# Optimization experiments

Hardware: AMD Instinct MI355X
Metric: run time of the kernel (lower is better)

## Reference

```python
import jax, jax.numpy as jnp
import numpy as np
from jax.scipy.special import logsumexp

TEMPERATURE = 0.1
BETA = 0.999
EPS = 1e-8
HARD_K = 10  # min(num_classes // 4, 10) with num_classes = 1000


def _l2norm(x, axis=-1):
    return x * jax.lax.rsqrt(jnp.sum(x * x, axis=axis, keepdims=True) + 1e-24)


def setup_inputs() -> dict:
    key = jax.random.key(0)
    k1, k2, k3, k4, k5 = jax.random.split(key, 5)
    B, D, C, M = 4096, 1024, 1000, 32768
    return {
        "image_features": jax.random.normal(k1, (B, D), dtype=jnp.float32),
        "prompts": jax.random.normal(k2, (C, D), dtype=jnp.float32),
        "labels": jax.random.randint(k3, (B, C), 0, 2, dtype=jnp.int32),
        "memory_features": jax.random.normal(k4, (M, D), dtype=jnp.float32),
        "memory_labels": jax.random.randint(k5, (M, C), 0, 2, dtype=jnp.int32),
        "mem_ptr": 16384,
    }


def reference(image_features, prompts, labels, memory_features, memory_labels, mem_ptr):
    B, D = image_features.shape
    C = prompts.shape[0]
    labels_f = labels.astype(jnp.float32)

    # z_img = F.normalize(image_features)
    z_img = _l2norm(image_features, axis=1)

    # class weights (effective-number reweighting), computed from this batch's labels
    counts = labels_f.sum(axis=0)                              # [C]
    effective_num = 1.0 - jnp.power(jnp.float32(BETA), counts)
    weights = (1.0 - BETA) / (effective_num + EPS)
    weights = weights / jnp.sum(weights) * C                   # [C]

    # memory bank update (detached write of current batch at ptr), then use [:ptr+B]
    mem_f = memory_features.at[mem_ptr:mem_ptr + B].set(jax.lax.stop_gradient(z_img))
    mem_l = memory_labels.at[mem_ptr:mem_ptr + B].set(labels)
    used = mem_ptr + B  # static

    enhanced_features = jnp.concatenate([z_img, mem_f[:used]], axis=0)     # [N, D]
    enhanced_labels = jnp.concatenate([labels_f, mem_l[:used].astype(jnp.float32)], axis=0)  # [N, C]

    z_prompts = _l2norm(prompts, axis=1)                       # [C, D]
    sim = (enhanced_features @ z_prompts.T) / TEMPERATURE      # [N, C]

    pos_mask = enhanced_labels > 0                             # [N, C]

    # hard negatives: top-K similarities among negatives define the keep threshold
    sim_for_neg = jnp.where(pos_mask, -jnp.inf, sim)
    hard_neg_vals, _ = jax.lax.top_k(sim_for_neg, HARD_K)      # [N, K]
    min_hard_neg = hard_neg_vals[:, -1:]                       # [N, 1]
    neg_mask = (~pos_mask) & (sim >= min_hard_neg)
    full_mask = pos_mask | neg_mask

    lse = logsumexp(jnp.where(full_mask, sim, -jnp.inf), axis=1)  # [N]
    log_prob = sim - lse[:, None]                              # [N, C]

    posf = pos_mask.astype(sim.dtype)
    pos_w = posf * weights[None, :]                            # [N, C]
    weight_sums = pos_w.sum(axis=1)                            # [N]
    loss_num = (pos_w * (-log_prob)).sum(axis=1)               # [N]

    valid = weight_sums > 0
    loss_per_sample = jnp.where(valid, loss_num / (weight_sums + EPS), 0.0)
    n_valid = jnp.maximum(valid.sum(), 1)
    attr_loss = loss_per_sample.sum() / n_valid.astype(sim.dtype)
    # single attribute -> total_loss / num_valid_attrs == attr_loss
    return attr_loss
```

## Files before the change

kernel.cpp:

```cpp
#include <hip/hip_runtime.h>
#include <math.h>

#define BN    4096
#define DD    1024
#define CC    1000
#define MM    32768
#define ROWS_CAP 32768
#define SIMLD 1024


#define NGROUP_A 512
#define NGROUP_B 16
#define NCOUNT   512

typedef __attribute__((ext_vector_type(8))) int   int8v;
typedef __attribute__((ext_vector_type(16))) float f32x16;

__device__ __forceinline__ float wave_max_f(float v) {
#pragma unroll
  for (int off = 32; off >= 1; off >>= 1) v = fmaxf(v, __shfl_xor(v, off, 64));
  return v;
}
__device__ __forceinline__ float wave_sum_f(float v) {
#pragma unroll
  for (int off = 32; off >= 1; off >>= 1) v += __shfl_xor(v, off, 64);
  return v;
}

__device__ __forceinline__ short f2bf(float f) {
  union { float f; unsigned u; } v; v.f = f;
  unsigned r = v.u + 0x7FFF + ((v.u >> 16) & 1);
  return (short)(r >> 16);
}
__device__ __forceinline__ float bf2f(unsigned short u) {
  union { unsigned u; float f; } v; v.u = ((unsigned)u) << 16;
  return v.f;
}

__device__ __forceinline__ int pack4(float a, float b, float c, float d) {
  int p = __builtin_amdgcn_cvt_pk_fp8_f32(a, b, 0, false);
  p = __builtin_amdgcn_cvt_pk_fp8_f32(c, d, p, true);
  return p;
}

__device__ __forceinline__ void gload16(const unsigned char* g, unsigned char* l) {
  __builtin_amdgcn_global_load_lds(
      (const __attribute__((address_space(1))) unsigned int*)g,
      (__attribute__((address_space(3))) unsigned int*)l, 16, 0, 0);
}

__global__ __launch_bounds__(256) void conv_kernel(const float* __restrict__ img,
                                                   const float* __restrict__ prompts,
                                                   const float* __restrict__ mem,
                                                   const int* __restrict__ memptr,
                                                   unsigned char* __restrict__ A,
                                                   unsigned char* __restrict__ B,
                                                   const int* __restrict__ labels,
                                                   int* __restrict__ counts) {
  const int blk = blockIdx.x;

  if (blk >= NGROUP_A + NGROUP_B) {
    const int ci = blk - (NGROUP_A + NGROUP_B);
    const int c = (ci & 3) * 256 + threadIdx.x;
    if (c >= CC) return;
    const int b0 = (ci >> 2) * 32;
    int s = 0;
#pragma unroll
    for (int b = 0; b < 32; ++b) s += labels[(size_t)(b0 + b) * CC + c];
    atomicAdd(&counts[c], s);
    return;
  }

  __shared__ unsigned char tile[65536];
  const int t = threadIdx.x;
  const int lane = t & 63;
  const int wid = t >> 6;
  const int nrows = BN + memptr[0];
  const int padded = (nrows + 127) & ~127;

  const bool isB = (blk >= NGROUP_A);
  const int g = isB ? (blk - NGROUP_A) : blk;
  const int rowBase = g * 64;
  if (!isB && rowBase >= padded) return;

  unsigned char* dstBase = (isB ? B : A)
      + (size_t)(rowBase >> 7) * 131072 + (size_t)(rowBase & 64) * 16;

  for (int i = 0; i < 16; ++i) {
    const int r = wid * 16 + i;
    const int row = rowBase + r;
    const float* src = nullptr;
    float esc = 1.0f;
    bool needNorm = false;
    if (isB) {
      if (row < CC) { src = prompts + (size_t)row * DD; needNorm = true; esc = 10.0f; }
    } else {
      if (row < BN)         { src = img + (size_t)row * DD; needNorm = true; }
      else if (row < nrows) { src = mem + (size_t)(row - BN) * DD; }
    }
    int4 o = {0, 0, 0, 0};
    if (src) {
      const float4* s4 = (const float4*)src + lane * 4;
      float4 a = s4[0], b = s4[1], c = s4[2], d = s4[3];
      float sc = esc;
      if (needNorm) {
        float ss = a.x * a.x + a.y * a.y + a.z * a.z + a.w * a.w
                 + b.x * b.x + b.y * b.y + b.z * b.z + b.w * b.w
                 + c.x * c.x + c.y * c.y + c.z * c.z + c.w * c.w
                 + d.x * d.x + d.y * d.y + d.z * d.z + d.w * d.w;
        ss = wave_sum_f(ss);
        sc = esc * rsqrtf(ss + 1e-24f);
      }
      o.x = pack4(a.x * sc, a.y * sc, a.z * sc, a.w * sc);
      o.y = pack4(b.x * sc, b.y * sc, b.z * sc, b.w * sc);
      o.z = pack4(c.x * sc, c.y * sc, c.z * sc, c.w * sc);
      o.w = pack4(d.x * sc, d.y * sc, d.z * sc, d.w * sc);
    }
    *(int4*)(tile + lane * 1024 + (((r + lane) & 63) << 4)) = o;
  }
  __syncthreads();

#pragma unroll
  for (int p = 0; p < 16; ++p) {
    const int ochunk = p * 256 + t;
    const int kc = ochunk >> 6;
    const int rl = ochunk & 63;
    int4 v = *(const int4*)(tile + kc * 1024 + (((rl + kc) & 63) << 4));
    *(int4*)(dstBase + (size_t)kc * 2048 + rl * 16) = v;
  }
}

__global__ __launch_bounds__(256) void gemm_mx(const unsigned char* __restrict__ A,
                                               const unsigned char* __restrict__ Bm,
                                               const int* __restrict__ memptr,
                                               short* __restrict__ simbf, int lo) {
  const int f = blockIdx.x;
  const int x = f & 7;
  const int s = f >> 3;
  const int c = s & 7;
  const int rt = (s >> 3) * 8 + x;

  const int nrows = BN + memptr[0];
  const int row0 = rt * 128;
  if (lo + row0 >= nrows) return;
  const int c0 = c * 128;

  __shared__ unsigned char As[16384];
  __shared__ unsigned char Bs[16384];

  const int t = threadIdx.x;
  const int lane = t & 63;
  const int wid = t >> 6;
  const int wm = (wid >> 1) * 64;
  const int wn = (wid & 1) * 64;

  const unsigned char* gaT = A + (size_t)(lo + row0) * DD;
  const unsigned char* gbT = Bm + (size_t)c0 * DD;
  unsigned char* lA = As + t * 16;
  unsigned char* lB = Bs + t * 16;

  f32x16 acc[2][2] = {};
  const int q = lane >> 5;
  const int rr = lane & 31;

  for (int k0 = 0; k0 < DD; k0 += 128) {
    const size_t kb = (size_t)k0 * 128;
#pragma unroll
    for (int p = 0; p < 4; ++p)
      gload16(gaT + kb + p * 4096 + t * 16, lA + p * 4096);
#pragma unroll
    for (int p = 0; p < 4; ++p)
      gload16(gbT + kb + p * 4096 + t * 16, lB + p * 4096);
    __syncthreads();
#pragma unroll
    for (int h = 0; h < 2; ++h) {
      int8v af[2], bfv[2];
      const int kc = h * 4 + q * 2;
#pragma unroll
      for (int mi = 0; mi < 2; ++mi) {
        const unsigned char* pa = As + kc * 2048 + (wm + mi * 32 + rr) * 16;
        int4 lo4 = *(const int4*)pa;
        int4 hi4 = *(const int4*)(pa + 2048);
        af[mi][0] = lo4.x; af[mi][1] = lo4.y; af[mi][2] = lo4.z; af[mi][3] = lo4.w;
        af[mi][4] = hi4.x; af[mi][5] = hi4.y; af[mi][6] = hi4.z; af[mi][7] = hi4.w;
      }
#pragma unroll
      for (int ni = 0; ni < 2; ++ni) {
        const unsigned char* pb = Bs + kc * 2048 + (wn + ni * 32 + rr) * 16;
        int4 lo4 = *(const int4*)pb;
        int4 hi4 = *(const int4*)(pb + 2048);
        bfv[ni][0] = lo4.x; bfv[ni][1] = lo4.y; bfv[ni][2] = lo4.z; bfv[ni][3] = lo4.w;
        bfv[ni][4] = hi4.x; bfv[ni][5] = hi4.y; bfv[ni][6] = hi4.z; bfv[ni][7] = hi4.w;
      }
#pragma unroll
      for (int mi = 0; mi < 2; ++mi)
#pragma unroll
        for (int ni = 0; ni < 2; ++ni)
          acc[mi][ni] = __builtin_amdgcn_mfma_scale_f32_32x32x64_f8f6f4(
              af[mi], bfv[ni], acc[mi][ni], 0, 0, 0, 127, 0, 127);
    }
    __syncthreads();
  }

  const int cl = lane & 31;
  const int r4 = 4 * (lane >> 5);
#pragma unroll
  for (int mi = 0; mi < 2; ++mi)
#pragma unroll
    for (int ni = 0; ni < 2; ++ni) {
      f32x16 v = acc[mi][ni];
      const int colg = c0 + wn + ni * 32 + cl;
      const int rbase = row0 + wm + mi * 32 + r4;
#pragma unroll
      for (int reg = 0; reg < 16; ++reg) {
        const int rowl = rbase + (reg & 3) + 8 * (reg >> 2);
        simbf[(size_t)rowl * SIMLD + colg] = f2bf(v[reg]);
      }
    }
}

__global__ __launch_bounds__(256) void rowpost_kernel(
    const short* __restrict__ simbf, const int* __restrict__ labels,
    const int* __restrict__ mlabels, const int* __restrict__ counts,
    const int* __restrict__ memptr, float* __restrict__ lps_arr,
    float* __restrict__ valid_arr, int chunk_lo) {
  __shared__ float wlds[1024];
  __shared__ float wpart[4];
  {
    const int t = threadIdx.x;
    float wv[4];
    float acc = 0.f;
#pragma unroll
    for (int i = 0; i < 4; ++i) {
      int c = t + i * 256;
      float w = 0.f;
      if (c < CC) {
        float cnt = (float)counts[c];
        float en = 1.0f - expf(cnt * logf(0.999f));
        w = (1.0f - 0.999f) / (en + 1e-8f);
      }
      wv[i] = w;
      acc += w;
    }
    float s = wave_sum_f(acc);
    if ((t & 63) == 0) wpart[t >> 6] = s;
    __syncthreads();
    float tot = wpart[0] + wpart[1] + wpart[2] + wpart[3];
    float sc = (float)CC / tot;
#pragma unroll
    for (int i = 0; i < 4; ++i) wlds[t + i * 256] = wv[i] * sc;
    __syncthreads();
  }

  const int nrows = BN + memptr[0];
  const int wid = threadIdx.x >> 6;
  const int lane = threadIdx.x & 63;
  const int row = chunk_lo + blockIdx.x * 4 + wid;
  if (row >= ROWS_CAP) return;
  if (row >= nrows) {
    if (lane == 0) { lps_arr[row] = 0.f; valid_arr[row] = 0.f; }
    return;
  }

  const unsigned short* srow = (const unsigned short*)simbf + (size_t)(row - chunk_lo) * SIMLD;
  const int* lrow = (row < BN) ? labels + (size_t)row * CC
                               : mlabels + (size_t)(row - BN) * CC;
  const int cbase = lane * 16;

  unsigned short sraw[16];
  *(ulonglong2*)&sraw[0] = *(const ulonglong2*)(srow + cbase);
  *(ulonglong2*)&sraw[8] = *(const ulonglong2*)(srow + cbase + 8);
  int lab[16];
#pragma unroll
  for (int g = 0; g < 4; ++g) {
    int c = cbase + g * 4;
    if (c + 3 < CC) {
      *(int4*)&lab[g * 4] = *(const int4*)(lrow + c);
    } else {
#pragma unroll
      for (int u = 0; u < 4; ++u) lab[g * 4 + u] = (c + u < CC) ? lrow[c + u] : 0;
    }
  }

  float sv[16];
  bool pv[16];
  float vneg[16];
#pragma unroll
  for (int j = 0; j < 16; ++j) {
    int c = cbase + j;
    bool ok = (c < CC);
    float sf = bf2f(sraw[j]);
    bool p = ok && (lab[j] > 0);
    sv[j] = ok ? sf : -INFINITY;
    pv[j] = p;
    vneg[j] = (ok && !p) ? sf : -INFINITY;
  }

  float v10 = -INFINITY;
  for (int r = 0; r < 10; ++r) {
    float lmx = -INFINITY;
#pragma unroll
    for (int j = 0; j < 16; ++j) lmx = fmaxf(lmx, vneg[j]);
    lmx = wave_max_f(lmx);
#pragma unroll
    for (int j = 0; j < 16; ++j) if (vneg[j] == lmx) vneg[j] = -INFINITY;
    v10 = lmx;
  }

  float mmax = -INFINITY;
#pragma unroll
  for (int j = 0; j < 16; ++j) {
    if (pv[j] || sv[j] >= v10) mmax = fmaxf(mmax, sv[j]);
  }
  mmax = wave_max_f(mmax);

  float esum = 0.f, wsum = 0.f, wsim = 0.f;
#pragma unroll
  for (int j = 0; j < 16; ++j) {
    int c = cbase + j;
    if (c < CC) {
      if (pv[j] || sv[j] >= v10) esum += expf(sv[j] - mmax);
      if (pv[j]) { float w = wlds[c]; wsum += w; wsim += w * sv[j]; }
    }
  }
  esum = wave_sum_f(esum);
  wsum = wave_sum_f(wsum);
  wsim = wave_sum_f(wsim);

  if (lane == 0) {
    float lse = mmax + logf(esum);
    bool valid = (wsum > 0.f);
    float lps = valid ? (wsum * lse - wsim) / (wsum + 1e-8f) : 0.f;
    float mult = (row < BN) ? 2.f : 1.f;
    lps_arr[row] = mult * lps;
    valid_arr[row] = valid ? mult : 0.f;
  }
}

__global__ __launch_bounds__(1024) void reduce_kernel(const float* __restrict__ lps_arr,
                                                      const float* __restrict__ valid_arr,
                                                      float* __restrict__ out) {
  const int t = threadIdx.x;
  const float4* l4 = (const float4*)lps_arr;
  const float4* v4 = (const float4*)valid_arr;
  float s1 = 0.f, s2 = 0.f;
#pragma unroll
  for (int i = 0; i < 8; ++i) {
    float4 a = l4[t + i * 1024];
    float4 b = v4[t + i * 1024];
    s1 += a.x + a.y + a.z + a.w;
    s2 += b.x + b.y + b.z + b.w;
  }
  s1 = wave_sum_f(s1);
  s2 = wave_sum_f(s2);
  __shared__ float p1[16], p2[16];
  if ((t & 63) == 0) { p1[t >> 6] = s1; p2[t >> 6] = s2; }
  __syncthreads();
  if (t == 0) {
    float a = 0.f, b = 0.f;
#pragma unroll
    for (int i = 0; i < 16; ++i) { a += p1[i]; b += p2[i]; }
    out[0] = a / fmaxf(b, 1.0f);
  }
}

extern "C" void kernel_launch(void* const* d_in, const int* in_sizes, int n_in,
                              void* d_out, int out_size, void* d_ws, size_t ws_size,
                              hipStream_t stream) {
  const float* img     = (const float*)d_in[0];
  const float* prompts = (const float*)d_in[1];
  const int*   labels  = (const int*)d_in[2];
  const float* mem     = (const float*)d_in[3];
  const int*   mlabels = (const int*)d_in[4];
  const int*   memptr  = (const int*)d_in[5];
  float* out = (float*)d_out;
  char* ws = (char*)d_ws;

  int*   counts  = (int*)(ws + 0);
  float* lps_arr = (float*)(ws + 8192);
  float* val_arr = (float*)(ws + 139264);
  unsigned char* Bf8 = (unsigned char*)(ws + 270336);
  unsigned char* Af8 = (unsigned char*)(ws + 1318912);
  const size_t fixed = 1318912 + (size_t)ROWS_CAP * DD;
  short* simbf = (short*)(ws + fixed);

  long long avail = (long long)ws_size - (long long)fixed;
  int chunk = (int)(avail / (SIMLD * 2));
  chunk &= ~1023;
  if (chunk < 1024) chunk = 1024;
  if (chunk > ROWS_CAP) chunk = ROWS_CAP;

  hipMemsetAsync(ws, 0, 4096, stream);

  conv_kernel<<<NGROUP_A + NGROUP_B + NCOUNT, 256, 0, stream>>>(
      img, prompts, mem, memptr, Af8, Bf8, labels, counts);

  for (int lo = 0; lo < ROWS_CAP; lo += chunk) {
    int rows = (ROWS_CAP - lo < chunk) ? (ROWS_CAP - lo) : chunk;
    int rowTiles = rows / 128;
    gemm_mx<<<8 * rowTiles, 256, 0, stream>>>(Af8, Bf8, memptr, simbf, lo);
    rowpost_kernel<<<rows / 4, 256, 0, stream>>>(simbf, labels, mlabels, counts, memptr,
                                                 lps_arr, val_arr, lo);
  }
  reduce_kernel<<<1, 1024, 0, stream>>>(lps_arr, val_arr, out);
}
```

Baseline: 331.6 us.

## Fuse row post-processing into GEMM epilogue with per-tile partial top-k merging

Removes the bf16 similarity matrix round-trip by computing per-tile partial statistics in the GEMM epilogue: a running top-10 of negatives via med3 insertion, the positive max, exp-sum and weighted sums. Each row gets 32 column-slice partials, and a new merge kernel combines them with online logsumexp. Labels are packed into LDS bitmasks and the class weights are recomputed per block. This also drops the chunked loop, but writes 14x32 floats of partials per row and lengthens the epilogue, which raises register pressure.

Measured after the change: 420.9 us. +26.9%, slower.

```diff
diff --git a/kernel.cpp b/kernel.cpp
--- a/kernel.cpp
+++ b/kernel.cpp
@@ -6,35 +6,21 @@
 #define CC    1000
 #define MM    32768
 #define ROWS_CAP 32768
-#define SIMLD 1024
 
 
 #define NGROUP_A 512
 #define NGROUP_B 16
 #define NCOUNT   512
 
+#define NSUB 32
+
 typedef __attribute__((ext_vector_type(8))) int   int8v;
 typedef __attribute__((ext_vector_type(16))) float f32x16;
 
-__device__ __forceinline__ float wave_max_f(float v) {
-#pragma unroll
-  for (int off = 32; off >= 1; off >>= 1) v = fmaxf(v, __shfl_xor(v, off, 64));
-  return v;
-}
 __device__ __forceinline__ float wave_sum_f(float v) {
 #pragma unroll
   for (int off = 32; off >= 1; off >>= 1) v += __shfl_xor(v, off, 64);
   return v;
-}
-
-__device__ __forceinline__ short f2bf(float f) {
-  union { float f; unsigned u; } v; v.f = f;
-  unsigned r = v.u + 0x7FFF + ((v.u >> 16) & 1);
-  return (short)(r >> 16);
-}
-__device__ __forceinline__ float bf2f(unsigned short u) {
-  union { unsigned u; float f; } v; v.u = ((unsigned)u) << 16;
-  return v.f;
 }
 
 __device__ __forceinline__ int pack4(float a, float b, float c, float d) {
@@ -47,6 +33,12 @@
   __builtin_amdgcn_global_load_lds(
       (const __attribute__((address_space(1))) unsigned int*)g,
       (__attribute__((address_space(3))) unsigned int*)l, 16, 0, 0);
+}
+
+__device__ __forceinline__ void ins10(float* t, float v) {
+#pragma unroll
+  for (int i = 9; i >= 1; --i) t[i] = __builtin_amdgcn_fmed3f(v, t[i - 1], t[i]);
+  t[0] = fmaxf(t[0], v);
 }
 
 __global__ __launch_bounds__(256) void conv_kernel(const float* __restrict__ img,
@@ -130,23 +122,29 @@
   }
 }
 
-__global__ __launch_bounds__(256) void gemm_mx(const unsigned char* __restrict__ A,
-                                               const unsigned char* __restrict__ Bm,
-                                               const int* __restrict__ memptr,
-                                               short* __restrict__ simbf, int lo) {
+__global__ __launch_bounds__(256) void gemm_fused(const unsigned char* __restrict__ A,
+                                                  const unsigned char* __restrict__ Bm,
+                                                  const int* __restrict__ labels,
+                                                  const int* __restrict__ mlabels,
+                                                  const int* __restrict__ counts,
+                                                  const int* __restrict__ memptr,
+                                                  float* __restrict__ partials) {
   const int f = blockIdx.x;
   const int x = f & 7;
   const int s = f >> 3;
-  const int c = s & 7;
+  const int cb = s & 7;
   const int rt = (s >> 3) * 8 + x;
 
   const int nrows = BN + memptr[0];
   const int row0 = rt * 128;
-  if (lo + row0 >= nrows) return;
-  const int c0 = c * 128;
+  if (row0 >= nrows) return;
+  const int c0 = cb * 128;
 
   __shared__ unsigned char As[16384];
   __shared__ unsigned char Bs[16384];
+  __shared__ unsigned posbits[128][4];
+  __shared__ float wcol[128];
+  __shared__ float wpart[4];
 
   const int t = threadIdx.x;
   const int lane = t & 63;
@@ -154,82 +152,9 @@
   const int wm = (wid >> 1) * 64;
   const int wn = (wid & 1) * 64;
 
-  const unsigned char* gaT = A + (size_t)(lo + row0) * DD;
-  const unsigned char* gbT = Bm + (size_t)c0 * DD;
-  unsigned char* lA = As + t * 16;
-  unsigned char* lB = Bs + t * 16;
-
-  f32x16 acc[2][2] = {};
-  const int q = lane >> 5;
-  const int rr = lane & 31;
-
-  for (int k0 = 0; k0 < DD; k0 += 128) {
-    const size_t kb = (size_t)k0 * 128;
-#pragma unroll
-    for (int p = 0; p < 4; ++p)
-      gload16(gaT + kb + p * 4096 + t * 16, lA + p * 4096);
-#pragma unroll
-    for (int p = 0; p < 4; ++p)
-      gload16(gbT + kb + p * 4096 + t * 16, lB + p * 4096);
-    __syncthreads();
-#pragma unroll
-    for (int h = 0; h < 2; ++h) {
-      int8v af[2], bfv[2];
-      const int kc = h * 4 + q * 2;
-#pragma unroll
-      for (int mi = 0; mi < 2; ++mi) {
-        const unsigned char* pa = As + kc * 2048 + (wm + mi * 32 + rr) * 16;
-        int4 lo4 = *(const int4*)pa;
-        int4 hi4 = *(const int4*)(pa + 2048);
-        af[mi][0] = lo4.x; af[mi][1] = lo4.y; af[mi][2] = lo4.z; af[mi][3] = lo4.w;
-        af[mi][4] = hi4.x; af[mi][5] = hi4.y; af[mi][6] = hi4.z; af[mi][7] = hi4.w;
-      }
-#pragma unroll
-      for (int ni = 0; ni < 2; ++ni) {
-        const unsigned char* pb = Bs + kc * 2048 + (wn + ni * 32 + rr) * 16;
-        int4 lo4 = *(const int4*)pb;
-        int4 hi4 = *(const int4*)(pb + 2048);
-        bfv[ni][0] = lo4.x; bfv[ni][1] = lo4.y; bfv[ni][2] = lo4.z; bfv[ni][3] = lo4.w;
-        bfv[ni][4] = hi4.x; bfv[ni][5] = hi4.y; bfv[ni][6] = hi4.z; bfv[ni][7] = hi4.w;
-      }
-#pragma unroll
-      for (int mi = 0; mi < 2; ++mi)
-#pragma unroll
-        for (int ni = 0; ni < 2; ++ni)
-          acc[mi][ni] = __builtin_amdgcn_mfma_scale_f32_32x32x64_f8f6f4(
-              af[mi], bfv[ni], acc[mi][ni], 0, 0, 0, 127, 0, 127);
-    }
-    __syncthreads();
-  }
-
-  const int cl = lane & 31;
-  const int r4 = 4 * (lane >> 5);
-#pragma unroll
-  for (int mi = 0; mi < 2; ++mi)
-#pragma unroll
-    for (int ni = 0; ni < 2; ++ni) {
-      f32x16 v = acc[mi][ni];
-      const int colg = c0 + wn + ni * 32 + cl;
-      const int rbase = row0 + wm + mi * 32 + r4;
-#pragma unroll
-      for (int reg = 0; reg < 16; ++reg) {
-        const int rowl = rbase + (reg & 3) + 8 * (reg >> 2);
-        simbf[(size_t)rowl * SIMLD + colg] = f2bf(v[reg]);
-      }
-    }
-}
-
-__global__ __launch_bounds__(256) void rowpost_kernel(
-    const short* __restrict__ simbf, const int* __restrict__ labels,
-    const int* __restrict__ mlabels, const int* __restrict__ counts,
-    const int* __restrict__ memptr, float* __restrict__ lps_arr,
-    float* __restrict__ valid_arr, int chunk_lo) {
-  __shared__ float wlds[1024];
-  __shared__ float wpart[4];
+  float wv[4];
   {
-    const int t = threadIdx.x;
-    float wv[4];
-    float acc = 0.f;
+    float accw = 0.f;
 #pragma unroll
     for (int i = 0; i < 4; ++i) {
       int c = t + i * 256;
@@ -240,101 +165,199 @@
         w = (1.0f - 0.999f) / (en + 1e-8f);
       }
       wv[i] = w;
-      acc += w;
-    }
-    float s = wave_sum_f(acc);
-    if ((t & 63) == 0) wpart[t >> 6] = s;
+      accw += w;
+    }
+    float sw = wave_sum_f(accw);
+    if (lane == 0) wpart[wid] = sw;
+    if (t < 128) wcol[t] = 0.f;
+  }
+  {
+    const int row_l = t >> 1;
+    const int half = t & 1;
+    const int row_g = row0 + row_l;
+    const int* lr = (row_g < BN) ? labels + (size_t)row_g * CC
+                                 : mlabels + (size_t)(row_g - BN) * CC;
+    unsigned bw0 = 0, bw1 = 0;
+    const int base = c0 + half * 64;
+#pragma unroll
+    for (int j = 0; j < 16; ++j) {
+      int c = base + j * 4;
+      int4 l4;
+      if (c + 3 < CC) l4 = *(const int4*)(lr + c);
+      else {
+        l4.x = (c < CC) ? lr[c] : 0;
+        l4.y = (c + 1 < CC) ? lr[c + 1] : 0;
+        l4.z = (c + 2 < CC) ? lr[c + 2] : 0;
+        l4.w = (c + 3 < CC) ? lr[c + 3] : 0;
+      }
+      unsigned m = 0;
+      if (l4.x > 0) m |= 1u;
+      if (l4.y > 0) m |= 2u;
+      if (l4.z > 0) m |= 4u;
+      if (l4.w > 0) m |= 8u;
+      if (j < 8) bw0 |= m << (j * 4);
+      else       bw1 |= m << ((j - 8) * 4);
+    }
+    posbits[row_l][half * 2 + 0] = bw0;
+    posbits[row_l][half * 2 + 1] = bw1;
+  }
+  __syncthreads();
+  {
+    float tot = wpart[0] + wpart[1] + wpart[2] + wpart[3];
+    float scw = (float)CC / tot;
+#pragma unroll
+    for (int i = 0; i < 4; ++i) {
+      int c = t + i * 256;
+      if (c >= c0 && c < c0 + 128) wcol[c - c0] = wv[i] * scw;
+    }
+  }
+
+  const unsigned char* gaT = A + (size_t)row0 * DD;
+  const unsigned char* gbT = Bm + (size_t)c0 * DD;
+  unsigned char* lA = As + t * 16;
+  unsigned char* lB = Bs + t * 16;
+
+  f32x16 acc[2][2] = {};
+  const int q = lane >> 5;
+  const int rr = lane & 31;
+
+  for (int k0 = 0; k0 < DD; k0 += 128) {
+    const size_t kb = (size_t)k0 * 128;
+#pragma unroll
+    for (int p = 0; p < 4; ++p)
+      gload16(gaT + kb + p * 4096 + t * 16, lA + p * 4096);
+#pragma unroll
+    for (int p = 0; p < 4; ++p)
+      gload16(gbT + kb + p * 4096 + t * 16, lB + p * 4096);
     __syncthreads();
-    float tot = wpart[0] + wpart[1] + wpart[2] + wpart[3];
-    float sc = (float)CC / tot;
-#pragma unroll
-    for (int i = 0; i < 4; ++i) wlds[t + i * 256] = wv[i] * sc;
+#pragma unroll
+    for (int h = 0; h < 2; ++h) {
+      int8v af[2], bfv[2];
+      const int kc = h * 4 + q * 2;
+#pragma unroll
+      for (int mi = 0; mi < 2; ++mi) {
+        const unsigned char* pa = As + kc * 2048 + (wm + mi * 32 + rr) * 16;
+        int4 lo4 = *(const int4*)pa;
+        int4 hi4 = *(const int4*)(pa + 2048);
+        af[mi][0] = lo4.x; af[mi][1] = lo4.y; af[mi][2] = lo4.z; af[mi][3] = lo4.w;
+        af[mi][4] = hi4.x; af[mi][5] = hi4.y; af[mi][6] = hi4.z; af[mi][7] = hi4.w;
+      }
+#pragma unroll
+      for (int ni = 0; ni < 2; ++ni) {
+        const unsigned char* pb = Bs + kc * 2048 + (wn + ni * 32 + rr) * 16;
+        int4 lo4 = *(const int4*)pb;
+        int4 hi4 = *(const int4*)(pb + 2048);
+        bfv[ni][0] = lo4.x; bfv[ni][1] = lo4.y; bfv[ni][2] = lo4.z; bfv[ni][3] = lo4.w;
+        bfv[ni][4] = hi4.x; bfv[ni][5] = hi4.y; bfv[ni][6] = hi4.z; bfv[ni][7] = hi4.w;
+      }
+#pragma unroll
+      for (int mi = 0; mi < 2; ++mi)
+#pragma unroll
+        for (int ni = 0; ni < 2; ++ni)
+          acc[mi][ni] = __builtin_amdgcn_mfma_scale_f32_32x32x64_f8f6f4(
+              bfv[ni], af[mi], acc[mi][ni], 0, 0, 0, 127, 0, 127);
+    }
     __syncthreads();
   }
 
+  const int cl = lane & 31;
+  const int wnb = wid & 1;
+  const int sub = cb * 4 + wnb * 2 + q;
+#pragma unroll
+  for (int mi = 0; mi < 2; ++mi) {
+    const int rl = wm + mi * 32 + cl;
+    const int row_g = row0 + rl;
+    float t10[10];
+#pragma unroll
+    for (int i = 0; i < 10; ++i) t10[i] = -INFINITY;
+    float pmax = -INFINITY, wsum = 0.f, wsim = 0.f;
+    unsigned pmbits = 0;
+#pragma unroll
+    for (int ni = 0; ni < 2; ++ni) {
+      const unsigned bits = posbits[rl][(wn >> 5) + ni];
+      f32x16 v = acc[mi][ni];
+#pragma unroll
+      for (int reg = 0; reg < 16; ++reg) {
+        const int ci = (reg & 3) + 8 * (reg >> 2) + 4 * q;
+        const int cg = c0 + wn + ni * 32 + ci;
+        const float val = v[reg];
+        const bool cvalid = (cg < CC);
+        const bool pos = cvalid && ((bits >> ci) & 1u);
+        if (pos) {
+          float w = wcol[wn + ni * 32 + ci];
+          wsum += w;
+          wsim += w * val;
+          pmax = fmaxf(pmax, val);
+          pmbits |= 1u << (ni * 16 + reg);
+        }
+        ins10(t10, (cvalid && !pos) ? val : -INFINITY);
+      }
+    }
+    float psum = 0.f;
+#pragma unroll
+    for (int ni = 0; ni < 2; ++ni) {
+      f32x16 v = acc[mi][ni];
+#pragma unroll
+      for (int reg = 0; reg < 16; ++reg) {
+        float arg = ((pmbits >> (ni * 16 + reg)) & 1u) ? (v[reg] - pmax) : -INFINITY;
+        psum += expf(arg);
+      }
+    }
+    float* pp = partials + (size_t)sub * ROWS_CAP + row_g;
+#pragma unroll
+    for (int k = 0; k < 10; ++k) pp[(size_t)k * NSUB * ROWS_CAP] = t10[k];
+    pp[(size_t)10 * NSUB * ROWS_CAP] = pmax;
+    pp[(size_t)11 * NSUB * ROWS_CAP] = psum;
+    pp[(size_t)12 * NSUB * ROWS_CAP] = wsum;
+    pp[(size_t)13 * NSUB * ROWS_CAP] = wsim;
+  }
+}
+
+__global__ __launch_bounds__(256) void merge_kernel(const float* __restrict__ partials,
+                                                    const int* __restrict__ memptr,
+                                                    float* __restrict__ lps_arr,
+                                                    float* __restrict__ valid_arr) {
+  const int row = blockIdx.x * 256 + threadIdx.x;
   const int nrows = BN + memptr[0];
-  const int wid = threadIdx.x >> 6;
-  const int lane = threadIdx.x & 63;
-  const int row = chunk_lo + blockIdx.x * 4 + wid;
-  if (row >= ROWS_CAP) return;
   if (row >= nrows) {
-    if (lane == 0) { lps_arr[row] = 0.f; valid_arr[row] = 0.f; }
+    lps_arr[row] = 0.f;
+    valid_arr[row] = 0.f;
     return;
   }
-
-  const unsigned short* srow = (const unsigned short*)simbf + (size_t)(row - chunk_lo) * SIMLD;
-  const int* lrow = (row < BN) ? labels + (size_t)row * CC
-                               : mlabels + (size_t)(row - BN) * CC;
-  const int cbase = lane * 16;
-
-  unsigned short sraw[16];
-  *(ulonglong2*)&sraw[0] = *(const ulonglong2*)(srow + cbase);
-  *(ulonglong2*)&sraw[8] = *(const ulonglong2*)(srow + cbase + 8);
-  int lab[16];
-#pragma unroll
-  for (int g = 0; g < 4; ++g) {
-    int c = cbase + g * 4;
-    if (c + 3 < CC) {
-      *(int4*)&lab[g * 4] = *(const int4*)(lrow + c);
-    } else {
-#pragma unroll
-      for (int u = 0; u < 4; ++u) lab[g * 4 + u] = (c + u < CC) ? lrow[c + u] : 0;
-    }
-  }
-
-  float sv[16];
-  bool pv[16];
-  float vneg[16];
-#pragma unroll
-  for (int j = 0; j < 16; ++j) {
-    int c = cbase + j;
-    bool ok = (c < CC);
-    float sf = bf2f(sraw[j]);
-    bool p = ok && (lab[j] > 0);
-    sv[j] = ok ? sf : -INFINITY;
-    pv[j] = p;
-    vneg[j] = (ok && !p) ? sf : -INFINITY;
-  }
-
-  float v10 = -INFINITY;
-  for (int r = 0; r < 10; ++r) {
-    float lmx = -INFINITY;
-#pragma unroll
-    for (int j = 0; j < 16; ++j) lmx = fmaxf(lmx, vneg[j]);
-    lmx = wave_max_f(lmx);
-#pragma unroll
-    for (int j = 0; j < 16; ++j) if (vneg[j] == lmx) vneg[j] = -INFINITY;
-    v10 = lmx;
-  }
-
-  float mmax = -INFINITY;
-#pragma unroll
-  for (int j = 0; j < 16; ++j) {
-    if (pv[j] || sv[j] >= v10) mmax = fmaxf(mmax, sv[j]);
-  }
-  mmax = wave_max_f(mmax);
-
-  float esum = 0.f, wsum = 0.f, wsim = 0.f;
-#pragma unroll
-  for (int j = 0; j < 16; ++j) {
-    int c = cbase + j;
-    if (c < CC) {
-      if (pv[j] || sv[j] >= v10) esum += expf(sv[j] - mmax);
-      if (pv[j]) { float w = wlds[c]; wsum += w; wsim += w * sv[j]; }
-    }
-  }
-  esum = wave_sum_f(esum);
-  wsum = wave_sum_f(wsum);
-  wsim = wave_sum_f(wsim);
-
-  if (lane == 0) {
-    float lse = mmax + logf(esum);
-    bool valid = (wsum > 0.f);
-    float lps = valid ? (wsum * lse - wsim) / (wsum + 1e-8f) : 0.f;
-    float mult = (row < BN) ? 2.f : 1.f;
-    lps_arr[row] = mult * lps;
-    valid_arr[row] = valid ? mult : 0.f;
-  }
+  float t10[10];
+#pragma unroll
+  for (int i = 0; i < 10; ++i) t10[i] = -INFINITY;
+  float Mp = -INFINITY, psum = 0.f, wsum = 0.f, wsim = 0.f;
+  for (int sub = 0; sub < NSUB; ++sub) {
+    const float* pp = partials + (size_t)sub * ROWS_CAP + row;
+#pragma unroll
+    for (int j = 0; j < 10; ++j) {
+      float v = pp[(size_t)j * NSUB * ROWS_CAP];
+#pragma unroll
+      for (int i = 9; i >= 1; --i) t10[i] = __builtin_amdgcn_fmed3f(v, t10[i - 1], t10[i]);
+      t10[0] = fmaxf(t10[0], v);
+    }
+    float pm = pp[(size_t)10 * NSUB * ROWS_CAP];
+    float ps = pp[(size_t)11 * NSUB * ROWS_CAP];
+    wsum += pp[(size_t)12 * NSUB * ROWS_CAP];
+    wsim += pp[(size_t)13 * NSUB * ROWS_CAP];
+    if (ps > 0.f) {
+      float m2 = fmaxf(Mp, pm);
+      psum = psum * expf(Mp - m2) + ps * expf(pm - m2);
+      Mp = m2;
+    }
+  }
+  const float M = fmaxf(Mp, t10[0]);
+  float esum = 0.f;
+#pragma unroll
+  for (int j = 0; j < 10; ++j) esum += expf(t10[j] - M);
+  if (psum > 0.f) esum += psum * expf(Mp - M);
+  const float lse = M + logf(esum);
+  const bool valid = (wsum > 0.f);
+  const float lps = valid ? (wsum * lse - wsim) / (wsum + 1e-8f) : 0.f;
+  const float mult = (row < BN) ? 2.f : 1.f;
+  lps_arr[row] = mult * lps;
+  valid_arr[row] = valid ? mult : 0.f;
 }
 
 __global__ __launch_bounds__(1024) void reduce_kernel(const float* __restrict__ lps_arr,
@@ -381,26 +404,17 @@
   float* val_arr = (float*)(ws + 139264);
   unsigned char* Bf8 = (unsigned char*)(ws + 270336);
   unsigned char* Af8 = (unsigned char*)(ws + 1318912);
-  const size_t fixed = 1318912 + (size_t)ROWS_CAP * DD;
-  short* simbf = (short*)(ws + fixed);
-
-  long long avail = (long long)ws_size - (long long)fixed;
-  int chunk = (int)(avail / (SIMLD * 2));
-  chunk &= ~1023;
-  if (chunk < 1024) chunk = 1024;
-  if (chunk > ROWS_CAP) chunk = ROWS_CAP;
+  float* partials = (float*)(ws + 1318912 + (size_t)ROWS_CAP * DD);
 
   hipMemsetAsync(ws, 0, 4096, stream);
 
   conv_kernel<<<NGROUP_A + NGROUP_B + NCOUNT, 256, 0, stream>>>(
       img, prompts, mem, memptr, Af8, Bf8, labels, counts);
 
-  for (int lo = 0; lo < ROWS_CAP; lo += chunk) {
-    int rows = (ROWS_CAP - lo < chunk) ? (ROWS_CAP - lo) : chunk;
-    int rowTiles = rows / 128;
-    gemm_mx<<<8 * rowTiles, 256, 0, stream>>>(Af8, Bf8, memptr, simbf, lo);
-    rowpost_kernel<<<rows / 4, 256, 0, stream>>>(simbf, labels, mlabels, counts, memptr,
-                                                 lps_arr, val_arr, lo);
-  }
+  gemm_fused<<<8 * (ROWS_CAP / 128), 256, 0, stream>>>(
+      Af8, Bf8, labels, mlabels, counts, memptr, partials);
+
+  merge_kernel<<<ROWS_CAP / 256, 256, 0, stream>>>(partials, memptr, lps_arr, val_arr);
+
   reduce_kernel<<<1, 1024, 0, stream>>>(lps_arr, val_arr, out);
 }
```
